# Kernel optimization log

Measured on AMD Instinct MI355X. Metric: run time of the kernel, lower is better.

## Reference

```python
import jax, jax.numpy as jnp
import numpy as np

NODES_PER_GRAPH = 1430  # hard-coded stride in the original forward
GENE0 = 1421            # first gene node index per graph
N_HEADS = 9


def gcn_conv(x, W, b, src, dst, n):
    """PyG-style GCNConv: D^-1/2 (A+I) D^-1/2 X W + b (self-loops added)."""
    h = x @ W  # [N, out]
    ones = jnp.ones(src.shape, jnp.float32)
    deg = jax.ops.segment_sum(ones, dst, num_segments=n) + 1.0  # +1 self-loop
    dinv = jax.lax.rsqrt(deg)
    norm = dinv[src] * dinv[dst]  # [E]
    agg = jax.ops.segment_sum(norm[:, None] * h[src], dst, num_segments=n)
    agg = agg + (dinv * dinv)[:, None] * h  # self-loop contribution
    return agg + b


def setup_inputs() -> dict:
    key = jax.random.key(0)
    ks = jax.random.split(key, 8)
    n_graphs = 512
    n = NODES_PER_GRAPH * n_graphs  # 732160 nodes
    e = n * 8                        # avg degree 8
    x = jax.random.normal(ks[0], (n, 1), jnp.float32)
    edge_index = jax.random.randint(ks[1], (2, e), 0, n, jnp.int32)
    y = jnp.zeros((n_graphs * N_HEADS,), jnp.int32)  # only y.size(0) is used
    W1 = jax.random.normal(ks[2], (1, 16), jnp.float32) * 0.5
    b1 = jnp.zeros((16,), jnp.float32)
    W2 = jax.random.normal(ks[3], (16, 16), jnp.float32) * 0.25
    b2 = jnp.zeros((16,), jnp.float32)
    fw1 = jax.random.normal(ks[4], (N_HEADS, 16, 8), jnp.float32) * 0.25
    fb1 = jnp.zeros((N_HEADS, 8), jnp.float32)
    fw2 = jax.random.normal(ks[5], (N_HEADS, 8, 1), jnp.float32) * 0.35
    fb2 = jnp.zeros((N_HEADS, 1), jnp.float32)
    return {"x": x, "edge_index": edge_index, "y": y, "W1": W1, "b1": b1,
            "W2": W2, "b2": b2, "fw1": fw1, "fb1": fb1, "fw2": fw2, "fb2": fb2}


def reference(x, edge_index, y, W1, b1, W2, b2, fw1, fb1, fw2, fb2):
    n = x.shape[0]
    src, dst = edge_index[0], edge_index[1]
    h = jax.nn.relu(gcn_conv(x, W1, b1, src, dst, n))
    # F.dropout(p=0.4) treated as identity (deterministic eval reference)
    h = jax.nn.relu(gcn_conv(h, W2, b2, src, dst, n))
    n_graphs = y.shape[0] // N_HEADS
    # fused version of the per-gene gather loop: idx[g, k] = 1421+g + k*1430
    idx = (GENE0 + jnp.arange(N_HEADS)[:, None]
           + jnp.arange(n_graphs)[None, :] * NODES_PER_GRAPH)  # [9, G]
    g = h[idx]  # [9, G, 16]
    z = jax.nn.relu(jnp.einsum('gnf,gfh->gnh', g, fw1) + fb1[:, None, :])
    pred = jnp.einsum('gnh,gho->gno', z, fw2) + fb2[:, None, :]  # [9, G, 1]
    return tuple(pred[i] for i in range(N_HEADS))
```

## Files before the change

kernel.cpp:

```cpp
#include <hip/hip_runtime.h>

#define NODES 1430
#define GENE0 1421
#define NHEADS 9
#define HBINS 131072
#define HWORDS (HBINS / 8)
#define BHIST 1024
#define GMAX 64

__device__ __forceinline__ float frelu(float v) { return v > 0.f ? v : 0.f; }

__global__ __launch_bounds__(BHIST, 4)
void k_hist(const int* __restrict__ esrc, const int* __restrict__ edst,
            unsigned int* __restrict__ copies,
            int* __restrict__ gene_cnt, int* __restrict__ gene_src,
            unsigned int* __restrict__ flagw,
            int e, int K, int R) {
    __shared__ unsigned int lds[HWORDS];
    int id = blockIdx.x;
    int k, r;
    if ((K & 7) == 0) {
        int xcd = id & 7;
        int slot = id >> 3;
        int cin = slot / R;
        k = xcd * (K >> 3) + cin;
        r = slot - cin * R;
    } else {
        k = id / R;
        r = id - k * R;
    }
    const int tid = threadIdx.x;
    {
        uint4* l4 = (uint4*)lds;
        for (int w = tid; w < HWORDS / 4; w += BHIST) l4[w] = make_uint4(0, 0, 0, 0);
    }
    __syncthreads();

    const unsigned int lo = (unsigned int)r * HBINS;
    const int e4 = e >> 2;
    const int Q = (e4 + K - 1) / K;
    const int beg = k * Q;
    const int end = min(beg + Q, e4);
    const int4* ed4 = (const int4*)edst;
    const int len = (end > beg) ? (end - beg) : 0;
    const int quarter = len >> 2;

    auto proc = [&](int4 d4) {
#pragma unroll
        for (int c = 0; c < 4; c++) {
            unsigned int d = (unsigned int)((&d4.x)[c]);
            unsigned int rel = d - lo;
            if (rel < HBINS)
                atomicAdd(&lds[rel >> 3], 1u << ((rel & 7u) * 4u));
        }
    };

    for (int i = tid; i < quarter; i += BHIST) {
        int j1 = beg + i;
        int j2 = j1 + quarter;
        int j3 = j2 + quarter;
        int j4 = j3 + quarter;
        int4 a = ed4[j1];
        int4 b = ed4[j2];
        int4 cc = ed4[j3];
        int4 dd = ed4[j4];
        proc(a); proc(b); proc(cc); proc(dd);
    }
    for (int i = (quarter << 2) + tid; i < len; i += BHIST) {
        proc(ed4[beg + i]);
    }

    {
        int sbeg = beg + (int)(((long long)len * r) / R);
        int send = beg + (int)(((long long)len * (r + 1)) / R);
        for (int j = sbeg + tid; j < send; j += BHIST) {
            int4 d4 = ed4[j];
#pragma unroll
            for (int c = 0; c < 4; c++) {
                unsigned int d = (unsigned int)((&d4.x)[c]);
                unsigned int graph = d / NODES;
                unsigned int pos = d - graph * NODES;
                if (pos >= GENE0) {
                    int s = esrc[4 * j + c];
                    atomicOr(&flagw[(unsigned)s >> 5], 1u << (s & 31));
                    int g = (int)(graph * NHEADS + (pos - GENE0));
                    int p = atomicAdd(gene_cnt + g, 1);
                    if (p < GMAX) gene_src[(g << 6) + p] = s;
                }
            }
        }
    }

    if (k == 0) {
        for (int j = (e4 << 2) + tid; j < e; j += BHIST) {
            unsigned int d = (unsigned int)edst[j];
            unsigned int rel = d - lo;
            if (rel < HBINS)
                atomicAdd(&lds[rel >> 3], 1u << ((rel & 7u) * 4u));
            if (r == 0) {
                unsigned int graph = d / NODES;
                unsigned int pos = d - graph * NODES;
                if (pos >= GENE0) {
                    int s = esrc[j];
                    atomicOr(&flagw[(unsigned)s >> 5], 1u << (s & 31));
                    int g = (int)(graph * NHEADS + (pos - GENE0));
                    int p = atomicAdd(gene_cnt + g, 1);
                    if (p < GMAX) gene_src[(g << 6) + p] = s;
                }
            }
        }
    }
    __syncthreads();
    uint4* dst4 = (uint4*)(copies + ((size_t)k * R + r) * HWORDS);
    const uint4* l4 = (const uint4*)lds;
    for (int w = tid; w < HWORDS / 4; w += BHIST) dst4[w] = l4[w];
}

__global__ void k_reduce(const unsigned int* __restrict__ copies,
                         const float* __restrict__ x,
                         float2* __restrict__ dx, float* __restrict__ t,
                         unsigned int* __restrict__ flagw,
                         int n, int K, int Wtot) {
    int w = blockIdx.x * blockDim.x + threadIdx.x;
    if (w >= Wtot) return;
    const unsigned int M = 0x0F0F0F0Fu;
    unsigned int e0 = 0, o0 = 0, e1 = 0, o1 = 0, e2 = 0, o2 = 0, e3 = 0, o3 = 0;
    int k = 0;
    for (; k + 4 <= K; k += 4) {
        unsigned int u0 = copies[(size_t)(k + 0) * Wtot + w];
        unsigned int u1 = copies[(size_t)(k + 1) * Wtot + w];
        unsigned int u2 = copies[(size_t)(k + 2) * Wtot + w];
        unsigned int u3 = copies[(size_t)(k + 3) * Wtot + w];
        e0 += u0 & M; o0 += (u0 >> 4) & M;
        e1 += u1 & M; o1 += (u1 >> 4) & M;
        e2 += u2 & M; o2 += (u2 >> 4) & M;
        e3 += u3 & M; o3 += (u3 >> 4) & M;
    }
    for (; k < K; k++) {
        unsigned int u = copies[(size_t)k * Wtot + w];
        e0 += u & M; o0 += (u >> 4) & M;
    }
    unsigned int evn = e0 + e1 + e2 + e3;
    unsigned int odd = o0 + o1 + o2 + o3;
    int i0 = w << 3;
    float v[8];
#pragma unroll
    for (int b = 0; b < 4; b++) {
        v[2 * b]     = (float)((evn >> (8 * b)) & 0xFFu);
        v[2 * b + 1] = (float)((odd >> (8 * b)) & 0xFFu);
    }
#pragma unroll
    for (int b = 0; b < 8; b++) v[b] = rsqrtf(v[b] + 1.f);
    float4 z4 = {0.f, 0.f, 0.f, 0.f};
    if (i0 + 7 < n) {
        float4 xa = *(const float4*)(x + i0);
        float4 xb = *(const float4*)(x + i0 + 4);
        float4 p0 = {v[0], v[0] * xa.x, v[1], v[1] * xa.y};
        float4 p1 = {v[2], v[2] * xa.z, v[3], v[3] * xa.w};
        float4 p2 = {v[4], v[4] * xb.x, v[5], v[5] * xb.y};
        float4 p3 = {v[6], v[6] * xb.z, v[7], v[7] * xb.w};
        float4* dst = (float4*)(dx + i0);
        dst[0] = p0; dst[1] = p1; dst[2] = p2; dst[3] = p3;
        *(float4*)(t + i0) = z4;
        *(float4*)(t + i0 + 4) = z4;
    } else {
        for (int b = 0; b < 8; b++)
            if (i0 + b < n) {
                float xv = x[i0 + b];
                dx[i0 + b] = make_float2(v[b], v[b] * xv);
                t[i0 + b] = 0.f;
            }
    }
#pragma unroll
    for (int b = 0; b < 8; b++) {
        int i = i0 + b;
        if (i < n) {
            unsigned int graph = (unsigned int)i / NODES;
            unsigned int pos = (unsigned int)i - graph * NODES;
            if (pos >= GENE0) atomicOr(&flagw[(unsigned)i >> 5], 1u << (i & 31));
        }
    }
}

__global__ void k_l1_scatter(const int* __restrict__ esrc, const int* __restrict__ edst,
                             const float2* __restrict__ dx,
                             const unsigned int* __restrict__ flagw,
                             float* __restrict__ t, int e) {
    int q = blockIdx.x * blockDim.x + threadIdx.x;
    int e16 = e >> 4;
    if (q < e16) {
        const int4* ed4 = (const int4*)edst;
        const int4* es4 = (const int4*)esrc;
        int4 d0 = ed4[4 * q + 0];
        int4 d1 = ed4[4 * q + 1];
        int4 d2 = ed4[4 * q + 2];
        int4 d3 = ed4[4 * q + 3];
        int4 s0 = es4[4 * q + 0];
        int4 s1 = es4[4 * q + 1];
        int4 s2 = es4[4 * q + 2];
        int4 s3 = es4[4 * q + 3];
        auto scat = [&](int4 dd, int4 ss) {
#pragma unroll
            for (int c = 0; c < 4; c++) {
                int d = (&dd.x)[c];
                if ((flagw[(unsigned)d >> 5] >> (d & 31)) & 1u) {
                    int s = (&ss.x)[c];
                    atomicAdd(t + d, dx[s].y);
                }
            }
        };
        scat(d0, s0); scat(d1, s1); scat(d2, s2); scat(d3, s3);
    } else if (q == e16) {
        for (int j = e16 << 4; j < e; j++) {
            int d = edst[j];
            if (!((flagw[(unsigned)d >> 5] >> (d & 31)) & 1u)) continue;
            int s = esrc[j];
            atomicAdd(t + d, dx[s].y);
        }
    }
}

__global__ void k_gene_final(const int* __restrict__ gene_src,
                             const float* __restrict__ t, const float2* __restrict__ dx,
                             const float* __restrict__ W1, const float* __restrict__ b1,
                             const float* __restrict__ W2, const float* __restrict__ b2,
                             const float* __restrict__ fw1, const float* __restrict__ fb1,
                             const float* __restrict__ fw2, const float* __restrict__ fb2,
                             float* __restrict__ out, int NG, int G) {
    int wid = (blockIdx.x * blockDim.x + threadIdx.x) >> 6;
    int lane = threadIdx.x & 63;
    if (wid >= NG) return;
    int g = wid;
    int graph = g / NHEADS;
    int head = g - graph * NHEADS;
    int node = graph * NODES + GENE0 + head;
    const int c = lane & 15;
    const int slot = lane >> 4;

    float w1r[16], b1r[16], w2c[16];
#pragma unroll
    for (int kk = 0; kk < 16; kk++) {
        w1r[kk] = W1[kk];
        b1r[kk] = b1[kk];
        w2c[kk] = W2[kk * 16 + c];
    }
    float2 dn2 = dx[node];
    float tn = t[node];

    float acc = 0.f;
    const int base = g << 6;
    for (int i = slot; i < GMAX; i += 4) {
        int s = gene_src[base + i];
        if (s < 0) break;
        float2 ds2 = dx[s];
        float ts = t[s];
        float us = ds2.x * ts + ds2.x * ds2.y;
        float m = 0.f;
#pragma unroll
        for (int kk = 0; kk < 16; kk++)
            m += frelu(us * w1r[kk] + b1r[kk]) * w2c[kk];
        acc += ds2.x * m;
    }
    acc += __shfl_xor(acc, 16, 64);
    acc += __shfl_xor(acc, 32, 64);

    float dn = dn2.x;
    float un = dn * tn + dn * dn2.y;
    float h2 = 0.f;
#pragma unroll
    for (int kk = 0; kk < 16; kk++)
        h2 += frelu(un * w1r[kk] + b1r[kk]) * w2c[kk];
    float h = frelu(dn * acc + dn * dn * h2 + b2[c]);

    float hv[16];
#pragma unroll
    for (int c2 = 0; c2 < 16; c2++) hv[c2] = __shfl(h, c2, 64);

    int kk = lane & 7;
    float z = fb1[head * 8 + kk];
#pragma unroll
    for (int c2 = 0; c2 < 16; c2++) z += hv[c2] * fw1[head * 128 + c2 * 8 + kk];
    float term = frelu(z) * fw2[head * 8 + kk];
    term += __shfl_xor(term, 1, 64);
    term += __shfl_xor(term, 2, 64);
    term += __shfl_xor(term, 4, 64);
    if (lane == 0) out[head * G + graph] = fb2[head] + term;
}

extern "C" void kernel_launch(void* const* d_in, const int* in_sizes, int n_in,
                              void* d_out, int out_size, void* d_ws, size_t ws_size,
                              hipStream_t stream) {
    const float* x   = (const float*)d_in[0];
    const int*   ei  = (const int*)d_in[1];
    const float* W1  = (const float*)d_in[3];
    const float* b1  = (const float*)d_in[4];
    const float* W2  = (const float*)d_in[5];
    const float* b2  = (const float*)d_in[6];
    const float* fw1 = (const float*)d_in[7];
    const float* fb1 = (const float*)d_in[8];
    const float* fw2 = (const float*)d_in[9];
    const float* fb2 = (const float*)d_in[10];

    int n = in_sizes[0];
    int e = in_sizes[1] / 2;
    int G = in_sizes[2] / NHEADS;
    int NG = G * NHEADS;
    const int* esrc = ei;
    const int* edst = ei + e;

    char* ws = (char*)d_ws;
    size_t off = 0;
    auto alloc = [&](size_t bytes) {
        char* p = ws + off;
        off += (bytes + 255) & ~(size_t)255;
        return p;
    };
    int*   gene_cnt      = (int*)alloc((size_t)NG * 4);
    unsigned int* flagw  = (unsigned int*)alloc((size_t)((n + 31) / 32) * 4);
    size_t zero_bytes    = off;
    int*    gene_src     = (int*)alloc((size_t)NG * GMAX * 4);
    size_t ff_bytes      = (size_t)NG * GMAX * 4;
    float*  t            = (float*)alloc((size_t)n * 4);
    float2* dx           = (float2*)alloc((size_t)n * 8);
    size_t fixed         = off;

    int R = (n + HBINS - 1) / HBINS;
    size_t per_copy = (size_t)R * HWORDS * 4;
    int K = 80;
    if (fixed + (size_t)K * per_copy > ws_size) {
        size_t avail = (ws_size > fixed) ? (ws_size - fixed) : 0;
        int kfit = (int)(avail / per_copy);
        if (kfit >= 8) kfit &= ~7;
        K = kfit < 1 ? 1 : (kfit < K ? kfit : K);
    }
    unsigned int* copies = (unsigned int*)alloc((size_t)K * per_copy);
    (void)n_in; (void)out_size;

    hipMemsetAsync(d_ws, 0, zero_bytes, stream);
    hipMemsetAsync(gene_src, 0xFF, ff_bytes, stream);

    const int B = 256;
    k_hist<<<K * R, BHIST, 0, stream>>>(esrc, edst, copies, gene_cnt, gene_src,
                                        flagw, e, K, R);
    int Wtot = R * HWORDS;
    k_reduce<<<(Wtot + B - 1) / B, B, 0, stream>>>(copies, x, dx, t, flagw, n, K, Wtot);
    int e16b = (e >> 4) + 1;
    k_l1_scatter<<<(e16b + B - 1) / B, B, 0, stream>>>(esrc, edst, dx, flagw, t, e);
    int waves_blocks = (NG * 64 + B - 1) / B;
    k_gene_final<<<waves_blocks, B, 0, stream>>>(gene_src, t, dx,
                                                 W1, b1, W2, b2,
                                                 fw1, fb1, fw2, fb2,
                                                 (float*)d_out, NG, G);
}
```

Before: 179.0 us.

## Queue flagged edges in LDS before scatter and drop gene_src 0xFF memset

The layer-1 scatter now has each block read coalesced int4 edge chunks and append flagged (src,dst) pairs to an LDS queue. A second pass then does the dx gathers and atomic adds, aiming for better load coalescing and latency hiding. The gene_final kernel bounds its loop by gene_cnt instead of a -1 sentinel, which removes the 0xFF memset of gene_src. This adds LDS atomics and a block barrier, and relies on gene_cnt being accurate.

```diff
diff --git a/kernel.cpp b/kernel.cpp
--- a/kernel.cpp
+++ b/kernel.cpp
@@ -7,6 +7,7 @@
 #define HWORDS (HBINS / 8)
 #define BHIST 1024
 #define GMAX 64
+#define QCAP 2048
 
 __device__ __forceinline__ float frelu(float v) { return v > 0.f ? v : 0.f; }
 
@@ -182,45 +183,56 @@
     }
 }
 
-__global__ void k_l1_scatter(const int* __restrict__ esrc, const int* __restrict__ edst,
-                             const float2* __restrict__ dx,
-                             const unsigned int* __restrict__ flagw,
-                             float* __restrict__ t, int e) {
-    int q = blockIdx.x * blockDim.x + threadIdx.x;
-    int e16 = e >> 4;
-    if (q < e16) {
-        const int4* ed4 = (const int4*)edst;
-        const int4* es4 = (const int4*)esrc;
-        int4 d0 = ed4[4 * q + 0];
-        int4 d1 = ed4[4 * q + 1];
-        int4 d2 = ed4[4 * q + 2];
-        int4 d3 = ed4[4 * q + 3];
-        int4 s0 = es4[4 * q + 0];
-        int4 s1 = es4[4 * q + 1];
-        int4 s2 = es4[4 * q + 2];
-        int4 s3 = es4[4 * q + 3];
-        auto scat = [&](int4 dd, int4 ss) {
+__global__ __launch_bounds__(256, 8)
+void k_l1_scatter(const int* __restrict__ esrc, const int* __restrict__ edst,
+                  const float2* __restrict__ dx,
+                  const unsigned int* __restrict__ flagw,
+                  float* __restrict__ t, int e) {
+    __shared__ int2 q[QCAP];
+    __shared__ int qn;
+    const int tid = threadIdx.x;
+    if (tid == 0) qn = 0;
+    __syncthreads();
+
+    const int4* ed4 = (const int4*)edst;
+    const int4* es4 = (const int4*)esrc;
+    const int e4 = e >> 2;
+    const int g0 = blockIdx.x * 1024;
+#pragma unroll
+    for (int u = 0; u < 4; u++) {
+        int gi = g0 + u * 256 + tid;
+        if (gi < e4) {
+            int4 dd = ed4[gi];
+            int4 ss = es4[gi];
 #pragma unroll
             for (int c = 0; c < 4; c++) {
                 int d = (&dd.x)[c];
                 if ((flagw[(unsigned)d >> 5] >> (d & 31)) & 1u) {
-                    int s = (&ss.x)[c];
-                    atomicAdd(t + d, dx[s].y);
+                    int p = atomicAdd(&qn, 1);
+                    if (p < QCAP) q[p] = make_int2((&ss.x)[c], d);
+                    else atomicAdd(t + d, dx[(&ss.x)[c]].y);
                 }
             }
-        };
-        scat(d0, s0); scat(d1, s1); scat(d2, s2); scat(d3, s3);
-    } else if (q == e16) {
-        for (int j = e16 << 4; j < e; j++) {
+        }
+    }
+    if (blockIdx.x == 0) {
+        for (int j = (e4 << 2) + tid; j < e; j += 256) {
             int d = edst[j];
-            if (!((flagw[(unsigned)d >> 5] >> (d & 31)) & 1u)) continue;
-            int s = esrc[j];
-            atomicAdd(t + d, dx[s].y);
-        }
-    }
-}
-
-__global__ void k_gene_final(const int* __restrict__ gene_src,
+            if ((flagw[(unsigned)d >> 5] >> (d & 31)) & 1u) {
+                int s = esrc[j];
+                atomicAdd(t + d, dx[s].y);
+            }
+        }
+    }
+    __syncthreads();
+    int m = min(qn, QCAP);
+    for (int i = tid; i < m; i += 256) {
+        int2 sd = q[i];
+        atomicAdd(t + sd.y, dx[sd.x].y);
+    }
+}
+
+__global__ void k_gene_final(const int* __restrict__ gene_cnt, const int* __restrict__ gene_src,
                              const float* __restrict__ t, const float2* __restrict__ dx,
                              const float* __restrict__ W1, const float* __restrict__ b1,
                              const float* __restrict__ W2, const float* __restrict__ b2,
@@ -237,6 +249,8 @@
     const int c = lane & 15;
     const int slot = lane >> 4;
 
+    int cnt = min(gene_cnt[g], GMAX);
+
     float w1r[16], b1r[16], w2c[16];
 #pragma unroll
     for (int kk = 0; kk < 16; kk++) {
@@ -249,9 +263,8 @@
 
     float acc = 0.f;
     const int base = g << 6;
-    for (int i = slot; i < GMAX; i += 4) {
+    for (int i = slot; i < cnt; i += 4) {
         int s = gene_src[base + i];
-        if (s < 0) break;
         float2 ds2 = dx[s];
         float ts = t[s];
         float us = ds2.x * ts + ds2.x * ds2.y;
@@ -319,7 +332,6 @@
     unsigned int* flagw  = (unsigned int*)alloc((size_t)((n + 31) / 32) * 4);
     size_t zero_bytes    = off;
     int*    gene_src     = (int*)alloc((size_t)NG * GMAX * 4);
-    size_t ff_bytes      = (size_t)NG * GMAX * 4;
     float*  t            = (float*)alloc((size_t)n * 4);
     float2* dx           = (float2*)alloc((size_t)n * 8);
     size_t fixed         = off;
@@ -337,17 +349,16 @@
     (void)n_in; (void)out_size;
 
     hipMemsetAsync(d_ws, 0, zero_bytes, stream);
-    hipMemsetAsync(gene_src, 0xFF, ff_bytes, stream);
 
     const int B = 256;
     k_hist<<<K * R, BHIST, 0, stream>>>(esrc, edst, copies, gene_cnt, gene_src,
                                         flagw, e, K, R);
     int Wtot = R * HWORDS;
     k_reduce<<<(Wtot + B - 1) / B, B, 0, stream>>>(copies, x, dx, t, flagw, n, K, Wtot);
-    int e16b = (e >> 4) + 1;
-    k_l1_scatter<<<(e16b + B - 1) / B, B, 0, stream>>>(esrc, edst, dx, flagw, t, e);
+    int nblk = ((e >> 2) + 1023) / 1024;
+    k_l1_scatter<<<nblk, 256, 0, stream>>>(esrc, edst, dx, flagw, t, e);
     int waves_blocks = (NG * 64 + B - 1) / B;
-    k_gene_final<<<waves_blocks, B, 0, stream>>>(gene_src, t, dx,
+    k_gene_final<<<waves_blocks, B, 0, stream>>>(gene_cnt, gene_src, t, dx,
                                                  W1, b1, W2, b2,
                                                  fw1, fb1, fw2, fb2,
                                                  (float*)d_out, NG, G);
```

Result: no change. 177.5 us (-0.8%).
